# Optimization experiments

Hardware: AMD Instinct MI355X
Metric: run time of the kernel (lower is better)

The kernel has to match this reference:

```python
import jax, jax.numpy as jnp
import numpy as np
import math

T_SCALE = 99
FEAT_DIM = 400
BATCH = 2
C = 256
NH = 8
NS = 32
NSPB = 3
RATIO = 0.5
LOCAL_STEP = 33


def build_sample_mask(T=T_SCALE, ns=NS, nspb=NSPB, ratio=RATIO):
    # Vectorized port of _get_interp1d_mask. Flat layout: [time, (bin, start, end)].
    N = ns * nspb
    e_idx, s_idx = np.meshgrid(np.arange(T), np.arange(T), indexing='ij')
    valid = s_idx < e_idx
    starts_i = s_idx[valid].astype(np.int64)
    ends_i = e_idx[valid].astype(np.int64)
    starts = starts_i.astype(np.float64)
    ends = ends_i.astype(np.float64)
    center = ends - starts + 1.0
    xmin = starts - center * ratio
    plen = (ends + center * ratio) - xmin
    S = xmin[:, None] + (plen / (N - 1.0))[:, None] * np.arange(N)[None, :]  # [P, N]
    down = np.trunc(S).astype(np.int64)  # matches int(math.modf(s)[1]) (trunc toward 0)
    dec = S - down                       # can be negative when s < 0, as in the original
    up = np.ceil(S).astype(np.int64)
    bin_col = (np.arange(N) // nspb)[None, :] * (T * T) + (starts_i * T + ends_i)[:, None]
    M = np.zeros(T * ns * T * T, np.float64)
    vd = (down >= 0) & (down <= T - 1)
    np.add.at(M, (down * (ns * T * T) + bin_col)[vd], ((1.0 - dec) / nspb)[vd])
    vu = (up >= 0) & (up <= T - 1)
    np.add.at(M, (up * (ns * T * T) + bin_col)[vu], (dec / nspb)[vu])
    return M.reshape(T, ns * T * T).astype(np.float32)


def pos_ebb(scale, size):
    pos = jnp.arange(scale, dtype=jnp.float32)[:, None]
    div = jnp.exp(jnp.arange(0, size, 2, dtype=jnp.float32) * (-math.log(10000.0) / size))
    ang = pos * div
    # interleave sin (even) / cos (odd)
    return jnp.stack([jnp.sin(ang), jnp.cos(ang)], axis=-1).reshape(scale, size)


def layer_norm(x, g, b, eps=1e-5):
    mu = jnp.mean(x, -1, keepdims=True)
    var = jnp.mean((x - mu) ** 2, -1, keepdims=True)
    return (x - mu) * jax.lax.rsqrt(var + eps) * g + b


def mha(x, w_qkv, b_qkv, w_o, b_o, nh=NH):
    t, b, c = x.shape
    hd = c // nh
    q, k, v = jnp.split(x @ w_qkv.T + b_qkv, 3, axis=-1)
    q = q.reshape(t, b, nh, hd)
    k = k.reshape(t, b, nh, hd)
    v = v.reshape(t, b, nh, hd)
    att = jnp.einsum('qbhd,kbhd->bhqk', q, k) / math.sqrt(hd)
    att = jax.nn.softmax(att, axis=-1)
    o = jnp.einsum('bhqk,kbhd->qbhd', att, v).reshape(t, b, c)
    return o @ w_o.T + b_o


def encoder(x, p):
    # PyTorch post-norm TransformerEncoder (eval mode, dropout off) + final LayerNorm
    (qkv_w, qkv_b, o_w, o_b, l1_w, l1_b, l2_w, l2_b, n1_g, n1_b, n2_g, n2_b, nf_g, nf_b) = p
    for i in range(qkv_w.shape[0]):
        a = mha(x, qkv_w[i], qkv_b[i], o_w[i], o_b[i])
        x = layer_norm(x + a, n1_g[i], n1_b[i])
        f = jax.nn.relu(x @ l1_w[i].T + l1_b[i]) @ l2_w[i].T + l2_b[i]
        x = layer_norm(x + f, n2_g[i], n2_b[i])
    return layer_norm(x, nf_g, nf_b)


def conv1d(x, w, b, pad, groups=1):
    y = jax.lax.conv_general_dilated(x, w, (1,), [(pad, pad)],
                                     dimension_numbers=('NCH', 'OIH', 'NCH'),
                                     feature_group_count=groups)
    return y + b[None, :, None]


def conv2d(x, w, b, pad):
    y = jax.lax.conv_general_dilated(x, w, (1, 1), [(pad, pad), (pad, pad)],
                                     dimension_numbers=('NCHW', 'OIHW', 'NCHW'))
    return y + b[None, :, None, None]


def conv3d(x, w, b, stride):
    y = jax.lax.conv_general_dilated(x, w, stride, [(0, 0)] * 3,
                                     dimension_numbers=('NCDHW', 'OIDHW', 'NCDHW'))
    return y + b[None, :, None, None, None]


def _forward(x, cb_w, cb_b, tg_qkv_w, tg_qkv_b, tg_o_w, tg_o_b, tg_l1_w, tg_l1_b, tg_l2_w, tg_l2_b, tg_n1_g, tg_n1_b, tg_n2_g, tg_n2_b, tg_nf_g, tg_nf_b, tl_qkv_w, tl_qkv_b, tl_o_w, tl_o_b, tl_l1_w, tl_l1_b, tl_l2_w, tl_l2_b, tl_n1_g, tl_n1_b, tl_n2_g, tl_n2_b, tl_nf_g, tl_nf_b, s1_w, s1_b, s2_w, s2_b, c3_w, c3_b, p1_w, p1_b, p2_w, p2_b, p3_w, p3_b, sample_mask):
    B, _, T = x.shape
    base = jax.nn.relu(conv1d(x, cb_w, cb_b, pad=1, groups=4))  # [B,C,T]
    # local transformer on LOCAL_STEP-strided windows
    group = T // LOCAL_STEP
    tl_p = (tl_qkv_w, tl_qkv_b, tl_o_w, tl_o_b, tl_l1_w, tl_l1_b, tl_l2_w, tl_l2_b, tl_n1_g, tl_n1_b, tl_n2_g, tl_n2_b, tl_nf_g, tl_nf_b)
    feat = base.reshape(B, C, LOCAL_STEP, group).transpose(2, 3, 0, 1).reshape(LOCAL_STEP, B * group, C)
    feat = encoder(feat + pos_ebb(LOCAL_STEP, C)[:, None, :], tl_p)
    local = feat.reshape(LOCAL_STEP * group, B, C).transpose(1, 2, 0)  # [B,C,T]
    # global bidirectional transformer (shared weights, flipped second pass)
    tg_p = (tg_qkv_w, tg_qkv_b, tg_o_w, tg_o_b, tg_l1_w, tg_l1_b, tg_l2_w, tg_l2_b, tg_n1_g, tg_n1_b, tg_n2_g, tg_n2_b, tg_nf_g, tg_nf_b)
    g = base.transpose(2, 0, 1)  # [T,B,C]
    pe = pos_ebb(T, C)[:, None, :]
    f1 = encoder(g + pe, tg_p)
    f2 = encoder(g[::-1] + pe, tg_p)
    base2 = local + (f1 + f2[::-1]).transpose(1, 2, 0)  # [B,C,T]
    s = jax.nn.relu(conv1d(base2, s1_w, s1_b, pad=1, groups=4))
    start1 = jax.nn.sigmoid(conv1d(s, s2_w, s2_b, pad=0))[:, 0, :]  # [B,T]
    # boundary-matching layer: dense matmul against precomputed interp mask
    bm = jnp.matmul(base2, sample_mask).reshape(B, C, NS, T, T)
    p = jax.nn.relu(conv3d(bm, c3_w, c3_b, (NS, 1, 1)))[:, :, 0]  # [B,C,T,T]
    p = jax.nn.relu(conv2d(p, p1_w, p1_b, pad=1))
    p = jax.nn.relu(conv2d(p, p2_w, p2_b, pad=1))
    cm = jax.nn.sigmoid(conv2d(p, p3_w, p3_b, pad=0))  # [B,2,T,T]
    return cm, start1


def setup_inputs() -> dict:
    key = jax.random.key(0)
    ks = iter(jax.random.split(key, 80))
    def rnd(shape):
        return 0.02 * jax.random.normal(next(ks), shape, dtype=jnp.float32)
    inp = {'x': jax.random.normal(next(ks), (BATCH, FEAT_DIM, T_SCALE), dtype=jnp.float32)}
    inp['cb_w'] = rnd((C, FEAT_DIM // 4, 3)); inp['cb_b'] = jnp.zeros((C,), jnp.float32)
    for pre, n in (('tg', 6), ('tl', 3)):
        inp[pre + '_qkv_w'] = rnd((n, 3 * C, C)); inp[pre + '_qkv_b'] = jnp.zeros((n, 3 * C), jnp.float32)
        inp[pre + '_o_w'] = rnd((n, C, C)); inp[pre + '_o_b'] = jnp.zeros((n, C), jnp.float32)
        inp[pre + '_l1_w'] = rnd((n, 1024, C)); inp[pre + '_l1_b'] = jnp.zeros((n, 1024), jnp.float32)
        inp[pre + '_l2_w'] = rnd((n, C, 1024)); inp[pre + '_l2_b'] = jnp.zeros((n, C), jnp.float32)
        inp[pre + '_n1_g'] = jnp.ones((n, C), jnp.float32); inp[pre + '_n1_b'] = jnp.zeros((n, C), jnp.float32)
        inp[pre + '_n2_g'] = jnp.ones((n, C), jnp.float32); inp[pre + '_n2_b'] = jnp.zeros((n, C), jnp.float32)
        inp[pre + '_nf_g'] = jnp.ones((C,), jnp.float32); inp[pre + '_nf_b'] = jnp.zeros((C,), jnp.float32)
    inp['s1_w'] = rnd((C, C // 4, 3)); inp['s1_b'] = jnp.zeros((C,), jnp.float32)
    inp['s2_w'] = rnd((1, C, 1)); inp['s2_b'] = jnp.zeros((1,), jnp.float32)
    inp['c3_w'] = rnd((C, C, NS, 1, 1)); inp['c3_b'] = jnp.zeros((C,), jnp.float32)
    inp['p1_w'] = rnd((C, C, 3, 3)); inp['p1_b'] = jnp.zeros((C,), jnp.float32)
    inp['p2_w'] = rnd((C, C, 3, 3)); inp['p2_b'] = jnp.zeros((C,), jnp.float32)
    inp['p3_w'] = rnd((2, C, 1, 1)); inp['p3_b'] = jnp.zeros((2,), jnp.float32)
    inp['sample_mask'] = jnp.asarray(build_sample_mask())  # [T, NS*T*T], exact BMN interp mask
    return inp


def reference(x, cb_w, cb_b, tg_qkv_w, tg_qkv_b, tg_o_w, tg_o_b, tg_l1_w, tg_l1_b, tg_l2_w, tg_l2_b, tg_n1_g, tg_n1_b, tg_n2_g, tg_n2_b, tg_nf_g, tg_nf_b, tl_qkv_w, tl_qkv_b, tl_o_w, tl_o_b, tl_l1_w, tl_l1_b, tl_l2_w, tl_l2_b, tl_n1_g, tl_n1_b, tl_n2_g, tl_n2_b, tl_nf_g, tl_nf_b, s1_w, s1_b, s2_w, s2_b, c3_w, c3_b, p1_w, p1_b, p2_w, p2_b, p3_w, p3_b, sample_mask):
    return _forward(x, cb_w, cb_b, tg_qkv_w, tg_qkv_b, tg_o_w, tg_o_b, tg_l1_w, tg_l1_b, tg_l2_w, tg_l2_b, tg_n1_g, tg_n1_b, tg_n2_g, tg_n2_b, tg_nf_g, tg_nf_b, tl_qkv_w, tl_qkv_b, tl_o_w, tl_o_b, tl_l1_w, tl_l1_b, tl_l2_w, tl_l2_b, tl_n1_g, tl_n1_b, tl_n2_g, tl_n2_b, tl_nf_g, tl_nf_b, s1_w, s1_b, s2_w, s2_b, c3_w, c3_b, p1_w, p1_b, p2_w, p2_b, p3_w, p3_b, sample_mask)
```

## Files before the change

kernel.cpp:

```cpp
#include <hip/hip_runtime.h>
#include <math.h>

#define T99   99
#define CC    256
#define NHH   8
#define FEAT  400
#define NS_   32
#define LSTEP 33

typedef __attribute__((ext_vector_type(8))) short s8v;
typedef __attribute__((ext_vector_type(4))) float f4v;

__device__ __forceinline__ void mfma_bf16(f4v& d, s8v a, s8v b) {
  asm("v_mfma_f32_16x16x32_bf16 %0, %1, %2, %0" : "+v"(d) : "v"(a), "v"(b));
}

__device__ __forceinline__ unsigned short f2bf(float f) {
  union { float f; unsigned u; } x; x.f = f;
  unsigned r = x.u + 0x7FFFu + ((x.u >> 16) & 1u);
  return (unsigned short)(r >> 16);
}
__device__ __forceinline__ float bf2f(unsigned short h) {
  union { unsigned u; float f; } x; x.u = ((unsigned)h) << 16;
  return x.f;
}
__device__ __forceinline__ float blo(unsigned u) { union { unsigned x; float f; } c; c.x = u << 16; return c.f; }
__device__ __forceinline__ float bhi(unsigned u) { union { unsigned x; float f; } c; c.x = u & 0xffff0000u; return c.f; }

__device__ __forceinline__ float pe_val(int pos, int c) {
  int i = c >> 1;
  float freq = expf((float)(2 * i) * (-0.03597789207803197f));
  float ang = (float)pos * freq;
  return (c & 1) ? cosf(ang) : sinf(ang);
}

__global__ __launch_bounds__(128) void k_convbase(const float* __restrict__ x,
                                                  const float* __restrict__ w,
                                                  const float* __restrict__ bias,
                                                  float* __restrict__ base) {
  int b = blockIdx.x >> 8, co = blockIdx.x & 255, t = threadIdx.x;
  if (t >= T99) return;
  int g = co >> 6;
  float acc = bias[co];
  const float* xp = x + (size_t)(b * FEAT + g * 100) * T99;
  const float* wp = w + (size_t)co * 300;
  for (int ic = 0; ic < 100; ++ic) {
    float x0 = (t > 0)  ? xp[ic * T99 + t - 1] : 0.f;
    float x1 = xp[ic * T99 + t];
    float x2 = (t < 98) ? xp[ic * T99 + t + 1] : 0.f;
    acc += wp[ic * 3] * x0 + wp[ic * 3 + 1] * x1 + wp[ic * 3 + 2] * x2;
  }
  base[(size_t)(b * CC + co) * T99 + t] = fmaxf(acc, 0.f);
}

struct PackP {
  const float *gq, *go, *g1, *g2;
  const float *lq, *lo, *l1, *l2;
  const float *c3w, *p1w, *p2w;
  unsigned short *wtg, *wtl, *wog, *wol, *w3, *wba, *wbb;
};
#define S0 4718592
#define S1 2359296
#define S2 393216
#define S3 196608
#define S4 2097152
#define S5 589824
#define S6 589824
#define STOT (S0+S1+S2+S3+S4+S5+S6)

__device__ __forceinline__ float convW_val(const float* qkv, const float* o, const float* l1,
                                           const float* l2, int idx) {
  int l = idx / 786432, r = idx % 786432;
  if (r < 196608)      return qkv[(size_t)l * 196608 + r];
  else if (r < 262144) return o[(size_t)l * 65536 + (r - 196608)];
  else if (r < 524288) return l1[(size_t)l * 262144 + (r - 262144)];
  else                 return l2[(size_t)l * 262144 + (r - 524288)];
}
__device__ __forceinline__ float wb2_val(const float* pw, int idx) {
  int v8 = idx >> 3, j = idx & 7;
  int lane = v8 & 63, cog = (v8 >> 6) & 15, kst = (v8 >> 10) & 7, tap = v8 >> 13;
  int co = cog * 16 + (lane & 15);
  int k  = kst * 32 + (lane >> 4) * 8;
  return pw[((size_t)co * 256 + k + j) * 9 + tap];
}

__global__ __launch_bounds__(256) void k_pack(PackP P) {
  for (int idx = blockIdx.x * 256 + threadIdx.x; idx < STOT; idx += gridDim.x * 256) {
    int r = idx;
    if (r < S0) { P.wtg[r] = f2bf(convW_val(P.gq, P.go, P.g1, P.g2, r)); continue; }
    r -= S0;
    if (r < S1) { P.wtl[r] = f2bf(convW_val(P.lq, P.lo, P.l1, P.l2, r)); continue; }
    r -= S1;
    if (r < S2) { int l = r >> 16, q = r & 65535; int ci = q >> 8, co = q & 255;
                  P.wog[r] = f2bf(P.go[(size_t)l * 65536 + co * 256 + ci]); continue; }
    r -= S2;
    if (r < S3) { int l = r >> 16, q = r & 65535; int ci = q >> 8, co = q & 255;
                  P.wol[r] = f2bf(P.lo[(size_t)l * 65536 + co * 256 + ci]); continue; }
    r -= S3;
    if (r < S4) { int ci = r & 255, co = (r >> 8) & 255, n = r >> 16;
                  P.w3[r] = f2bf(P.c3w[((size_t)(co << 8) + ci) * 32 + n]); continue; }
    r -= S4;
    if (r < S5) { P.wba[r] = f2bf(wb2_val(P.p1w, r)); continue; }
    r -= S5;
    P.wbb[r] = f2bf(wb2_val(P.p2w, r));
  }
}

__global__ __launch_bounds__(256) void k_build2(const float* __restrict__ base,
                                                float* __restrict__ xl, unsigned short* __restrict__ xlb,
                                                float* __restrict__ xg, unsigned short* __restrict__ xgb) {
  int tid = threadIdx.x;
  if (blockIdx.z == 0) {
    if (blockIdx.x >= 198) return;
    int idx = blockIdx.x * 256 + tid;
    int ls = idx / 1536, r = idx % 1536, j = r >> 8, c = r & 255;
    int g = j >> 1, b = j & 1, t = ls * 3 + g;
    float v = base[(size_t)(b * CC + c) * T99 + t] + pe_val(ls, c);
    xl[idx] = v; xlb[idx] = f2bf(v);
  } else {
    int idx = blockIdx.x * 256 + tid;
    int t = idx >> 10, r = idx & 1023, b4 = r >> 8, c = r & 255;
    float v = (b4 < 2) ? base[(size_t)(b4 * CC + c) * T99 + t]
                       : base[(size_t)((b4 - 2) * CC + c) * T99 + (98 - t)];
    v += pe_val(t, c);
    xg[idx] = v; xgb[idx] = f2bf(v);
  }
}

struct GJ {
  const unsigned short* Ab;
  const unsigned short* W;
  const float* bias;
  const float* R;
  float* Yf;
  unsigned short* Yb;
  int M, N, K, flags;
};

__device__ void g_body(const GJ& j, int m0, int n0) {
  __shared__ __align__(16) unsigned short Al[64][40];
  __shared__ __align__(16) unsigned short Bl[64][40];
  int tid = threadIdx.x;
  int lane = tid & 63, w = tid >> 6, wm = w >> 1, wn = w & 1;
  int sp = tid >> 2, kc = (tid & 3) << 3;
  f4v acc[2][2];
#pragma unroll
  for (int mt = 0; mt < 2; ++mt)
#pragma unroll
    for (int nt = 0; nt < 2; ++nt) acc[mt][nt] = (f4v){0.f, 0.f, 0.f, 0.f};

  for (int k0 = 0; k0 < j.K; k0 += 32) {
    s8v av = {0, 0, 0, 0, 0, 0, 0, 0};
    int row = m0 + sp;
    if (row < j.M) av = *(const s8v*)&j.Ab[(size_t)row * j.K + k0 + kc];
    *(s8v*)&Al[sp][kc] = av;
    *(s8v*)&Bl[sp][kc] = *(const s8v*)&j.W[(size_t)(n0 + sp) * j.K + k0 + kc];
    __syncthreads();
    s8v af[2], bf[2];
#pragma unroll
    for (int mt = 0; mt < 2; ++mt)
      af[mt] = *(const s8v*)&Al[wm * 32 + mt * 16 + (lane & 15)][(lane >> 4) * 8];
#pragma unroll
    for (int nt = 0; nt < 2; ++nt)
      bf[nt] = *(const s8v*)&Bl[wn * 32 + nt * 16 + (lane & 15)][(lane >> 4) * 8];
#pragma unroll
    for (int mt = 0; mt < 2; ++mt)
#pragma unroll
      for (int nt = 0; nt < 2; ++nt) mfma_bf16(acc[mt][nt], af[mt], bf[nt]);
    __syncthreads();
  }
  asm volatile("s_nop 7\n\ts_nop 7\n\ts_nop 4");
#pragma unroll
  for (int mt = 0; mt < 2; ++mt) {
#pragma unroll
    for (int nt = 0; nt < 2; ++nt) {
      int col = n0 + wn * 32 + nt * 16 + (lane & 15);
      float bv = j.bias[col];
#pragma unroll
      for (int r = 0; r < 4; ++r) {
        int row = m0 + wm * 32 + mt * 16 + (lane >> 4) * 4 + r;
        if (row < j.M) {
          float v = acc[mt][nt][r] + bv;
          if (j.flags & 2) v += j.R[(size_t)row * j.N + col];
          if (j.flags & 1) v = fmaxf(v, 0.f);
          if (!(j.flags & 8)) j.Yf[(size_t)row * j.N + col] = v;
          if (j.flags & 4) j.Yb[(size_t)row * j.N + col] = f2bf(v);
        }
      }
    }
  }
}

__global__ __launch_bounds__(256) void k_g(GJ j) {
  if ((int)blockIdx.x * 64 >= j.M) return;
  g_body(j, blockIdx.x * 64, blockIdx.y * 64);
}

__global__ __launch_bounds__(256) void k_g2(GJ j0, GJ j1) {
  if (blockIdx.z == 0) {
    if ((int)blockIdx.x * 64 >= j0.M) return;
    g_body(j0, blockIdx.x * 64, blockIdx.y * 64);
  } else {
    if ((int)blockIdx.x * 64 >= j1.M) return;
    g_body(j1, blockIdx.x * 64, blockIdx.y * 64);
  }
}

__device__ void apl_body(const unsigned short* __restrict__ qkvb,
                         const unsigned short* __restrict__ Wt,
                         const float* __restrict__ ob,
                         const float* __restrict__ g, const float* __restrict__ beta,
                         float* __restrict__ X, unsigned short* __restrict__ Xb,
                         int T_, int B_, int tok) {
  __shared__ float qrow[256];
  __shared__ float sc[8][100];
  __shared__ float den[8];
  __shared__ float att[256];
  __shared__ float rs[256], rq[256];
  int tid = threadIdx.x;
  int b = tok % B_;
  qrow[tid] = bf2f(qkvb[(size_t)tok * 768 + tid]);
  __syncthreads();
  for (int e = tid; e < 8 * T_; e += 256) {
    int h = e / T_, k = e % T_;
    const unsigned short* kp = qkvb + (size_t)(k * B_ + b) * 768 + 256 + h * 32;
    float d = 0.f;
#pragma unroll
    for (int i = 0; i < 32; ++i) d += qrow[h * 32 + i] * bf2f(kp[i]);
    sc[h][k] = d * 0.176776695296636881f;
  }
  __syncthreads();
  int h = tid >> 5, lane = tid & 31;
  float m = -1e30f;
  for (int k = lane; k < T_; k += 32) m = fmaxf(m, sc[h][k]);
#pragma unroll
  for (int msk = 16; msk >= 1; msk >>= 1) m = fmaxf(m, __shfl_xor(m, msk, 32));
  float sum = 0.f;
  for (int k = lane; k < T_; k += 32) {
    float p = expf(sc[h][k] - m);
    sc[h][k] = p; sum += p;
  }
#pragma unroll
  for (int msk = 16; msk >= 1; msk >>= 1) sum += __shfl_xor(sum, msk, 32);
  if (lane == 0) den[h] = sum;
  float o = 0.f;
  for (int k = 0; k < T_; ++k)
    o += sc[h][k] * bf2f(qkvb[(size_t)(k * B_ + b) * 768 + 512 + tid]);
  o /= den[h];
  att[tid] = o;
  __syncthreads();
  float acc = ob[tid];
#pragma unroll 8
  for (int ci = 0; ci < 256; ++ci) acc += att[ci] * bf2f(Wt[(size_t)ci * 256 + tid]);
  float v = acc + X[(size_t)tok * 256 + tid];
  rs[tid] = v; rq[tid] = v * v; __syncthreads();
  for (int oo = 128; oo > 0; oo >>= 1) { if (tid < oo) { rs[tid] += rs[tid + oo]; rq[tid] += rq[tid + oo]; } __syncthreads(); }
  float mu = rs[0] * (1.f / 256.f);
  float var = rq[0] * (1.f / 256.f) - mu * mu;
  float r = (v - mu) * rsqrtf(var + 1e-5f) * g[tid] + beta[tid];
  X[(size_t)tok * 256 + tid] = r;
  Xb[(size_t)tok * 256 + tid] = f2bf(r);
}

__global__ __launch_bounds__(256) void k_apl(const unsigned short* qkvb, const unsigned short* Wt,
                                             const float* ob, const float* g, const float* beta,
                                             float* X, unsigned short* Xb, int T_, int B_, int M) {
  if ((int)blockIdx.x >= M) return;
  apl_body(qkvb, Wt, ob, g, beta, X, Xb, T_, B_, blockIdx.x);
}

__global__ __launch_bounds__(256) void k_apl2(const unsigned short* q0, const unsigned short* Wt0,
                                              const float* ob0, const float* g0, const float* be0,
                                              float* X0, unsigned short* Xb0, int T0, int B0, int M0,
                                              const unsigned short* q1, const unsigned short* Wt1,
                                              const float* ob1, const float* g1, const float* be1,
                                              float* X1, unsigned short* Xb1, int T1, int B1, int M1) {
  int tok = blockIdx.x;
  if (blockIdx.z == 0) {
    if (tok >= M0) return;
    apl_body(q0, Wt0, ob0, g0, be0, X0, Xb0, T0, B0, tok);
  } else {
    if (tok >= M1) return;
    apl_body(q1, Wt1, ob1, g1, be1, X1, Xb1, T1, B1, tok);
  }
}

__device__ __forceinline__ void ln_body(const float* __restrict__ X, const float* __restrict__ g,
                                        const float* __restrict__ bb, float* __restrict__ Y,
                                        unsigned short* __restrict__ Yb, int tok) {
  __shared__ float rs[256], rq[256];
  int c = threadIdx.x;
  float v = X[(size_t)tok * 256 + c];
  rs[c] = v; rq[c] = v * v; __syncthreads();
  for (int o = 128; o > 0; o >>= 1) { if (c < o) { rs[c] += rs[c + o]; rq[c] += rq[c + o]; } __syncthreads(); }
  float mu = rs[0] * (1.f / 256.f);
  float var = rq[0] * (1.f / 256.f) - mu * mu;
  float r = (v - mu) * rsqrtf(var + 1e-5f) * g[c] + bb[c];
  Y[(size_t)tok * 256 + c] = r;
  if (Yb) Yb[(size_t)tok * 256 + c] = f2bf(r);
}

__global__ __launch_bounds__(256) void k_ln(const float* __restrict__ X, const float* __restrict__ g,
                                            const float* __restrict__ bb, float* __restrict__ Y,
                                            unsigned short* __restrict__ Yb) {
  ln_body(X, g, bb, Y, Yb, blockIdx.x);
}

__global__ __launch_bounds__(256) void k_ln2(const float* __restrict__ X0, const float* __restrict__ g0,
                                             const float* __restrict__ bb0, float* __restrict__ Y0,
                                             unsigned short* __restrict__ Yb0, int n0,
                                             const float* __restrict__ X1, const float* __restrict__ g1,
                                             const float* __restrict__ bb1, float* __restrict__ Y1,
                                             unsigned short* __restrict__ Yb1, int n1) {
  int tok = blockIdx.x;
  if (blockIdx.z == 0) { if (tok < n0) ln_body(X0, g0, bb0, Y0, Yb0, tok); }
  else                 { if (tok < n1) ln_body(X1, g1, bb1, Y1, Yb1, tok); }
}

__device__ __forceinline__ float ln3(float v, float* rs, float* rq) {
  int c = threadIdx.x;
  rs[c] = v; rq[c] = v * v; __syncthreads();
  for (int o = 128; o > 0; o >>= 1) { if (c < o) { rs[c] += rs[c + o]; rq[c] += rq[c + o]; } __syncthreads(); }
  float mu = rs[0] * (1.f / 256.f);
  float var = rq[0] * (1.f / 256.f) - mu * mu;
  float r = (v - mu) * rsqrtf(var + 1e-5f);
  __syncthreads();
  return r;
}

__global__ __launch_bounds__(256) void k_combine2(const float* __restrict__ XL, const float* __restrict__ XG,
                                                  const float* __restrict__ nfgL, const float* __restrict__ nfbL,
                                                  const float* __restrict__ nfgG, const float* __restrict__ nfbG,
                                                  float* __restrict__ base2, unsigned short* __restrict__ b2t) {
  __shared__ float rs[256], rq[256];
  int t = blockIdx.x % T99, b = blockIdx.x / T99, c = threadIdx.x;
  int ls = t / 3, g = t % 3;
  int tokL = ls * 6 + g * 2 + b;
  int tok1 = t * 4 + b;
  int tok2 = (98 - t) * 4 + 2 + b;
  float vL = ln3(XL[(size_t)tokL * 256 + c], rs, rq) * nfgL[c] + nfbL[c];
  float v1 = ln3(XG[(size_t)tok1 * 256 + c], rs, rq) * nfgG[c] + nfbG[c];
  float v2 = ln3(XG[(size_t)tok2 * 256 + c], rs, rq) * nfgG[c] + nfbG[c];
  float v = vL + v1 + v2;
  base2[((size_t)(b * CC) + c) * T99 + t] = v;
  b2t[((size_t)(b * T99) + t) * 256 + c] = f2bf(v);
}

__device__ void gm_body(const unsigned short* __restrict__ b2t, const unsigned short* __restrict__ w3tb,
                        unsigned short* __restrict__ Gb, int mi, int ni, int nb, bool padzero) {
  __shared__ __align__(16) unsigned short Al[64][40];
  __shared__ __align__(16) unsigned short Bl[64][40];
  int n = nb >> 1, b = nb & 1;
  int m0 = mi * 64, n0 = ni * 64;
  int tid = threadIdx.x;
  if (padzero)
    ((unsigned int*)(Gb + (size_t)NS_ * T99 * 512))[tid] = 0u;
  const unsigned short* A = b2t + (size_t)b * T99 * 256;
  const unsigned short* W = w3tb + (size_t)n * 65536;
  int lane = tid & 63, w = tid >> 6, wm = w >> 1, wn = w & 1;
  int sp = tid >> 2, kc = (tid & 3) << 3;
  f4v acc[2][2];
#pragma unroll
  for (int mt = 0; mt < 2; ++mt)
#pragma unroll
    for (int nt = 0; nt < 2; ++nt) acc[mt][nt] = (f4v){0.f, 0.f, 0.f, 0.f};
#pragma unroll
  for (int k0 = 0; k0 < 256; k0 += 32) {
    s8v av = {0, 0, 0, 0, 0, 0, 0, 0};
    int row = m0 + sp;
    if (row < T99) av = *(const s8v*)&A[(size_t)row * 256 + k0 + kc];
    *(s8v*)&Al[sp][kc] = av;
    *(s8v*)&Bl[sp][kc] = *(const s8v*)&W[(size_t)(n0 + sp) * 256 + k0 + kc];
    __syncthreads();
    s8v af[2], bf[2];
#pragma unroll
    for (int mt = 0; mt < 2; ++mt)
      af[mt] = *(const s8v*)&Al[wm * 32 + mt * 16 + (lane & 15)][(lane >> 4) * 8];
#pragma unroll
    for (int nt = 0; nt < 2; ++nt)
      bf[nt] = *(const s8v*)&Bl[wn * 32 + nt * 16 + (lane & 15)][(lane >> 4) * 8];
#pragma unroll
    for (int mt = 0; mt < 2; ++mt)
#pragma unroll
      for (int nt = 0; nt < 2; ++nt) mfma_bf16(acc[mt][nt], af[mt], bf[nt]);
    __syncthreads();
  }
  asm volatile("s_nop 7\n\ts_nop 7\n\ts_nop 4");
#pragma unroll
  for (int mt = 0; mt < 2; ++mt) {
#pragma unroll
    for (int nt = 0; nt < 2; ++nt) {
      int co = n0 + wn * 32 + nt * 16 + (lane & 15);
#pragma unroll
      for (int r = 0; r < 4; ++r) {
        int t = m0 + wm * 32 + mt * 16 + (lane >> 4) * 4 + r;
        if (t < T99)
          Gb[((size_t)(n * T99 + t) * 256 + co) * 2 + b] = f2bf(acc[mt][nt][r]);
      }
    }
  }
}

__device__ void sfuse_body(const float* __restrict__ base2, const float* __restrict__ s1w,
                           const float* __restrict__ s1b, const float* __restrict__ s2w,
                           const float* __restrict__ s2b, float* __restrict__ out, int bid) {
  __shared__ float rs[256];
  int b = bid / T99, t = bid % T99, co = threadIdx.x;
  int g = co >> 6;
  float acc = s1b[co];
  const float* xp = base2 + (size_t)(b * CC + g * 64) * T99;
  const float* wp = s1w + (size_t)co * 192;
  for (int ic = 0; ic < 64; ++ic) {
    float x0 = (t > 0)  ? xp[ic * T99 + t - 1] : 0.f;
    float x1 = xp[ic * T99 + t];
    float x2 = (t < 98) ? xp[ic * T99 + t + 1] : 0.f;
    acc += wp[ic * 3] * x0 + wp[ic * 3 + 1] * x1 + wp[ic * 3 + 2] * x2;
  }
  rs[co] = fmaxf(acc, 0.f) * s2w[co];
  __syncthreads();
  for (int o = 128; o > 0; o >>= 1) { if (co < o) rs[co] += rs[co + o]; __syncthreads(); }
  if (co == 0) out[bid] = 1.f / (1.f + expf(-(rs[0] + s2b[0])));
}

__global__ __launch_bounds__(256) void k_gmsf(const unsigned short* b2t, const unsigned short* w3tb,
                                              unsigned short* Gb,
                                              const float* base2, const float* s1w, const float* s1b,
                                              const float* s2w, const float* s2b, float* sout) {
  int bid = blockIdx.x;
  if (bid < 512) {
    int mi = bid & 1, ni = (bid >> 1) & 3, nb = bid >> 3;
    gm_body(b2t, w3tb, Gb, mi, ni, nb, bid == 0);
  } else {
    sfuse_body(base2, s1w, s1b, s2w, s2b, sout, bid - 512);
  }
}

__global__ __launch_bounds__(256) void k_ppre(const unsigned short* __restrict__ Gb,
                                              const float* __restrict__ c3b,
                                              unsigned int* __restrict__ pinb32) {
  __shared__ float w0s[96], w1s[96];
  __shared__ int   ofs[96];
  __shared__ float part[128][4];
  int e = blockIdx.x % T99, s = blockIdx.x / T99;
  int tid = threadIdx.x;
  if (s >= e) {
    if (tid < 128) {
      float z0 = fmaxf(c3b[2 * tid], 0.f), z1 = fmaxf(c3b[2 * tid + 1], 0.f);
      unsigned int zz = ((unsigned)f2bf(z1) << 16) | (unsigned)f2bf(z0);
      pinb32[((size_t)s * T99 + e) * 128 + tid] = zz;
      pinb32[((size_t)(T99 + s) * T99 + e) * 128 + tid] = zz;
    }
    return;
  }
  if (tid < 96) {
    double center = (double)(e - s + 1);
    double S = ((double)s - 0.5 * center) + ((2.0 * center - 1.0) / 95.0) * (double)tid;
    double dn = trunc(S);
    double dec = S - dn;
    int di = (int)dn;
    double uc = ceil(S);
    int ui = (int)uc;
    int n = tid / 3;
    float w0 = 0.f, w1 = 0.f;
    int r0 = 0;
    if (dn >= 0.0 && dn <= 98.0) {
      r0 = di;
      w0 = (float)((1.0 - dec) / 3.0);
      if (uc >= 0.0 && uc <= 98.0) {
        if (ui == di) w0 += (float)(dec / 3.0);
        else          w1  = (float)(dec / 3.0);
      }
    }
    w0s[tid] = w0; w1s[tid] = w1;
    ofs[tid] = (n * T99 + r0) * 1024;
  }
  __syncthreads();
  int ch = tid & 127, half = tid >> 7;
  float a00 = 0.f, a01 = 0.f, a10 = 0.f, a11 = 0.f;
  const char* basep = (const char*)Gb + ch * 8;
  int k0 = half * 48;
#pragma unroll 8
  for (int k = k0; k < k0 + 48; ++k) {
    float w0 = w0s[k], w1 = w1s[k];
    const uint2* p = (const uint2*)(basep + ofs[k]);
    uint2 u0 = p[0];
    uint2 u1 = p[128];
    a00 += w0 * blo(u0.x) + w1 * blo(u1.x);
    a01 += w0 * bhi(u0.x) + w1 * bhi(u1.x);
    a10 += w0 * blo(u0.y) + w1 * blo(u1.y);
    a11 += w0 * bhi(u0.y) + w1 * bhi(u1.y);
  }
  if (half) { part[ch][0] = a00; part[ch][1] = a01; part[ch][2] = a10; part[ch][3] = a11; }
  __syncthreads();
  if (tid < 128) {
    a00 += part[ch][0]; a01 += part[ch][1]; a10 += part[ch][2]; a11 += part[ch][3];
    float b0 = c3b[2 * tid], b1 = c3b[2 * tid + 1];
    unsigned int zb0 = ((unsigned)f2bf(fmaxf(a10 + b1, 0.f)) << 16) | (unsigned)f2bf(fmaxf(a00 + b0, 0.f));
    unsigned int zb1 = ((unsigned)f2bf(fmaxf(a11 + b1, 0.f)) << 16) | (unsigned)f2bf(fmaxf(a01 + b0, 0.f));
    pinb32[((size_t)s * T99 + e) * 128 + tid] = zb0;
    pinb32[((size_t)(T99 + s) * T99 + e) * 128 + tid] = zb1;
  }
}

__global__ __launch_bounds__(256) void k_cvec(const float* __restrict__ pw, const float* __restrict__ cin,
                                              const float* __restrict__ bias, int reluCin,
                                              float* __restrict__ coutF, unsigned short* __restrict__ coutB) {
  __shared__ float rs[256];
  int co = blockIdx.x, ci = threadIdx.x;
  float c = cin[ci];
  if (reluCin) c = fmaxf(c, 0.f);
  const float* wp = pw + ((size_t)co * 256 + ci) * 9;
  float wsum = 0.f;
#pragma unroll
  for (int t = 0; t < 9; ++t) wsum += wp[t];
  rs[ci] = wsum * c;
  __syncthreads();
  for (int o = 128; o > 0; o >>= 1) { if (ci < o) rs[ci] += rs[ci + o]; __syncthreads(); }
  if (ci == 0) {
    float r = fmaxf(bias[co] + rs[0], 0.f);
    coutF[co] = r;
    coutB[co] = f2bf(r);
  }
}

__device__ __forceinline__ int aoff(int s) {
  int tap = s >> 3, kst = s & 7;
  return ((tap / 3) * 10 + (tap % 3)) * 264 + kst * 32;
}
__device__ __forceinline__ void ldb4(const unsigned short* __restrict__ B0, int s, s8v* dst) {
#pragma unroll
  for (int nt = 0; nt < 4; ++nt) dst[nt] = *(const s8v*)(B0 + (size_t)s * 8192 + nt * 512);
}

__global__ __launch_bounds__(256) void k_conv3x3(const unsigned short* __restrict__ in,
                                                 const unsigned short* __restrict__ wbf,
                                                 const float* __restrict__ bias,
                                                 const unsigned short* __restrict__ cvecB,
                                                 int D, int lo, int hi,
                                                 unsigned short* __restrict__ out) {
  __shared__ __align__(16) unsigned short Ah[100 * 264];
  int b = blockIdx.z;
  int co0 = blockIdx.y * 128;
  int ti = blockIdx.x / 13, tj = blockIdx.x % 13;
  int i0 = ti * 8, j0 = tj * 8;
  int tid = threadIdx.x;

  if (i0 - 1 >= lo && i0 + 8 <= hi && j0 - 1 >= lo && j0 + 8 <= hi && i0 - 1 >= j0 + 8 + D) {
    const unsigned int* cv = (const unsigned int*)(cvecB + co0);
    unsigned int* ob = (unsigned int*)out;
#pragma unroll
    for (int r = 0; r < 16; ++r) {
      int idx = r * 256 + tid;
      int sp = idx >> 6, cp = idx & 63;
      int gi = i0 + (sp >> 3), gj = j0 + (sp & 7);
      ob[((size_t)(b * T99 + gi) * T99 + gj) * 128 + (co0 >> 1) + cp] = cv[cp];
    }
    return;
  }

#pragma unroll
  for (int it = 0; it < 13; ++it) {
    int chunk = it * 256 + tid;
    if (chunk < 3200) {
      int row = chunk >> 5;
      int cc = (chunk & 31) * 8;
      int gi = i0 + row / 10 - 1, gj = j0 + row % 10 - 1;
      s8v val = {0, 0, 0, 0, 0, 0, 0, 0};
      if (gi >= 0 && gi < T99 && gj >= 0 && gj < T99)
        val = *(const s8v*)&in[((size_t)(b * T99 + gi) * T99 + gj) * 256 + cc];
      *(s8v*)&Ah[row * 264 + cc] = val;
    }
  }
  __syncthreads();

  int lane = tid & 63, w = tid >> 6, wm = w >> 1, wn = w & 1;
  int l15 = lane & 15, lk = lane >> 4;
  int spL0 = wm * 32 + l15, spL1 = spL0 + 16;
  int hr0 = (spL0 >> 3) * 10 + (spL0 & 7);
  int hr1 = (spL1 >> 3) * 10 + (spL1 & 7);
  const unsigned short* A0 = &Ah[hr0 * 264 + lk * 8];
  const unsigned short* A1 = &Ah[hr1 * 264 + lk * 8];
  int cogbase = blockIdx.y * 8 + wn * 4;
  const unsigned short* B0 = wbf + (size_t)cogbase * 512 + (size_t)lane * 8;

  f4v acc[2][4];
#pragma unroll
  for (int mt = 0; mt < 2; ++mt)
#pragma unroll
    for (int nt = 0; nt < 4; ++nt) acc[mt][nt] = (f4v){0.f, 0.f, 0.f, 0.f};

  s8v a0c, a1c, a0n, a1n;
  s8v bq[3][4];
  a0c = *(const s8v*)(A0 + aoff(0));
  a1c = *(const s8v*)(A1 + aoff(0));
  a0n = a0c; a1n = a1c;
  ldb4(B0, 0, bq[0]);
  ldb4(B0, 1, bq[1]);
#pragma unroll
  for (int s = 0; s < 72; ++s) {
    if (s + 2 < 72) ldb4(B0, s + 2, bq[(s + 2) % 3]);
    if (s + 1 < 72) {
      a0n = *(const s8v*)(A0 + aoff(s + 1));
      a1n = *(const s8v*)(A1 + aoff(s + 1));
    }
#pragma unroll
    for (int nt = 0; nt < 4; ++nt) {
      mfma_bf16(acc[0][nt], a0c, bq[s % 3][nt]);
      mfma_bf16(acc[1][nt], a1c, bq[s % 3][nt]);
    }
    a0c = a0n; a1c = a1n;
  }

  asm volatile("s_nop 7\n\ts_nop 7\n\ts_nop 4");
#pragma unroll
  for (int mt = 0; mt < 2; ++mt) {
#pragma unroll
    for (int nt = 0; nt < 4; ++nt) {
      int co = co0 + wn * 64 + nt * 16 + l15;
      float bv = bias[co];
#pragma unroll
      for (int r = 0; r < 4; ++r) {
        int sp = wm * 32 + mt * 16 + lk * 4 + r;
        int gi = i0 + (sp >> 3), gj = j0 + (sp & 7);
        if (gi < T99 && gj < T99) {
          float v = fmaxf(acc[mt][nt][r] + bv, 0.f);
          out[((size_t)(b * T99 + gi) * T99 + gj) * 256 + co] = f2bf(v);
        }
      }
    }
  }
}

__global__ __launch_bounds__(256) void k_p3(const unsigned short* __restrict__ p2o,
                                            const float* __restrict__ w, const float* __restrict__ bias,
                                            float* __restrict__ cm) {
  int idx = blockIdx.x * 256 + threadIdx.x;
  if (idx >= 2 * T99 * T99) return;
  int j = idx % T99, i = (idx / T99) % T99, b = idx / (T99 * T99);
  float a0 = bias[0], a1 = bias[1];
  const unsigned short* row = p2o + ((size_t)(b * T99 + i) * T99 + j) * 256;
  for (int c8 = 0; c8 < 256; c8 += 8) {
    s8v v = *(const s8v*)&row[c8];
#pragma unroll
    for (int q = 0; q < 8; ++q) {
      float x = bf2f((unsigned short)v[q]);
      a0 += w[c8 + q] * x;
      a1 += w[256 + c8 + q] * x;
    }
  }
  size_t base = (size_t)b * 2 * T99 * T99 + (size_t)i * T99 + j;
  cm[base] = 1.f / (1.f + expf(-a0));
  cm[base + T99 * T99] = 1.f / (1.f + expf(-a1));
}

struct EncW {
  const float *qkvw, *qkvb, *ow, *ob, *l1w, *l1b, *l2w, *l2b, *n1g, *n1b, *n2g, *n2b, *nfg, *nfb;
};
struct EncBufs {
  float* x; unsigned short* xb;
  float* yb;
  unsigned short *qkvb, *hb;
  int M;
};

static GJ jqkv(const EncW& W, const unsigned short* Wb, int l, const EncBufs& B) {
  GJ j = {}; j.Ab = B.xb; j.W = Wb + (size_t)l * 786432;
  j.bias = W.qkvb + (size_t)l * 768; j.Yb = B.qkvb; j.flags = 4 | 8;
  j.M = B.M; j.N = 768; j.K = 256; return j;
}
static GJ jffn1(const EncW& W, const unsigned short* Wb, int l, const EncBufs& B) {
  GJ j = {}; j.Ab = B.xb; j.W = Wb + (size_t)l * 786432 + 262144;
  j.bias = W.l1b + (size_t)l * 1024; j.Yb = B.hb; j.flags = 1 | 4 | 8;
  j.M = B.M; j.N = 1024; j.K = 256; return j;
}
static GJ jffn2(const EncW& W, const unsigned short* Wb, int l, const EncBufs& B) {
  GJ j = {}; j.Ab = B.hb; j.W = Wb + (size_t)l * 786432 + 524288;
  j.bias = W.l2b + (size_t)l * 256; j.R = B.x; j.Yf = B.yb; j.flags = 2;
  j.M = B.M; j.N = 256; j.K = 1024; return j;
}

extern "C" void kernel_launch(void* const* d_in, const int* in_sizes, int n_in,
                              void* d_out, int out_size, void* d_ws, size_t ws_size,
                              hipStream_t stream) {
  (void)in_sizes; (void)n_in; (void)out_size; (void)ws_size;
  const float* x    = (const float*)d_in[0];
  const float* cbw  = (const float*)d_in[1];
  const float* cbb  = (const float*)d_in[2];
  EncW tg = {(const float*)d_in[3],  (const float*)d_in[4],  (const float*)d_in[5],  (const float*)d_in[6],
             (const float*)d_in[7],  (const float*)d_in[8],  (const float*)d_in[9],  (const float*)d_in[10],
             (const float*)d_in[11], (const float*)d_in[12], (const float*)d_in[13], (const float*)d_in[14],
             (const float*)d_in[15], (const float*)d_in[16]};
  EncW tl = {(const float*)d_in[17], (const float*)d_in[18], (const float*)d_in[19], (const float*)d_in[20],
             (const float*)d_in[21], (const float*)d_in[22], (const float*)d_in[23], (const float*)d_in[24],
             (const float*)d_in[25], (const float*)d_in[26], (const float*)d_in[27], (const float*)d_in[28],
             (const float*)d_in[29], (const float*)d_in[30]};
  const float* s1w = (const float*)d_in[31];
  const float* s1b = (const float*)d_in[32];
  const float* s2w = (const float*)d_in[33];
  const float* s2b = (const float*)d_in[34];
  const float* c3w = (const float*)d_in[35];
  const float* c3b = (const float*)d_in[36];
  const float* p1w = (const float*)d_in[37];
  const float* p1b = (const float*)d_in[38];
  const float* p2w = (const float*)d_in[39];
  const float* p2b = (const float*)d_in[40];
  const float* p3w = (const float*)d_in[41];
  const float* p3b = (const float*)d_in[42];

  float* outp = (float*)d_out;

  char* wp = (char*)d_ws;
  auto alloc = [&](size_t bytes) -> void* {
    void* p = (void*)wp;
    wp += (bytes + 255) & ~(size_t)255;
    return p;
  };
  float* base  = (float*)alloc(sizeof(float) * 2 * CC * T99);
  const int ML = 198, MG = 396;
  EncBufs BG, BL;
  BG.M = MG; BL.M = ML;
  BG.x  = (float*)alloc(sizeof(float) * MG * 256);
  BL.x  = (float*)alloc(sizeof(float) * ML * 256);
  BG.xb = (unsigned short*)alloc(sizeof(short) * MG * 256);
  BL.xb = (unsigned short*)alloc(sizeof(short) * ML * 256);
  BG.yb = (float*)alloc(sizeof(float) * MG * 256);
  BL.yb = (float*)alloc(sizeof(float) * ML * 256);
  BG.qkvb = (unsigned short*)alloc(sizeof(short) * MG * 768);
  BL.qkvb = (unsigned short*)alloc(sizeof(short) * ML * 768);
  BG.hb = (unsigned short*)alloc(sizeof(short) * MG * 1024);
  BL.hb = (unsigned short*)alloc(sizeof(short) * ML * 1024);
  float* base2 = (float*)alloc(sizeof(float) * 2 * CC * T99);
  unsigned short* b2t = (unsigned short*)alloc(sizeof(short) * 2 * T99 * 256);
  unsigned short* w3tb = (unsigned short*)alloc(sizeof(short) * 32 * 256 * 256);
  unsigned short* Gb = (unsigned short*)alloc(sizeof(short) * (2 * NS_ * T99 * 256 + 512));
  unsigned short* pinb = (unsigned short*)alloc(sizeof(short) * 2 * T99 * T99 * 256);
  unsigned short* p1o  = (unsigned short*)alloc(sizeof(short) * 2 * T99 * T99 * 256);
  unsigned short* p2o  = (unsigned short*)alloc(sizeof(short) * 2 * T99 * T99 * 256);
  unsigned short* wb2a = (unsigned short*)alloc(sizeof(short) * 9 * 256 * 256);
  unsigned short* wb2b = (unsigned short*)alloc(sizeof(short) * 9 * 256 * 256);
  unsigned short* wtgb = (unsigned short*)alloc(sizeof(short) * 6 * 786432);
  unsigned short* wtlb = (unsigned short*)alloc(sizeof(short) * 3 * 786432);
  unsigned short* wotg = (unsigned short*)alloc(sizeof(short) * 6 * 65536);
  unsigned short* wotl = (unsigned short*)alloc(sizeof(short) * 3 * 65536);
  float* c1F = (float*)alloc(sizeof(float) * 256);
  unsigned short* c1B = (unsigned short*)alloc(sizeof(short) * 256);
  float* c2F = (float*)alloc(sizeof(float) * 256);
  unsigned short* c2B = (unsigned short*)alloc(sizeof(short) * 256);

  PackP PK = {tg.qkvw, tg.ow, tg.l1w, tg.l2w, tl.qkvw, tl.ow, tl.l1w, tl.l2w,
              c3w, p1w, p2w, wtgb, wtlb, wotg, wotl, w3tb, wb2a, wb2b};
  k_pack<<<dim3(8192), dim3(256), 0, stream>>>(PK);
  k_cvec<<<dim3(256), dim3(256), 0, stream>>>(p1w, c3b, p1b, 1, c1F, c1B);
  k_cvec<<<dim3(256), dim3(256), 0, stream>>>(p2w, c1F, p2b, 0, c2F, c2B);
  k_convbase<<<dim3(512), dim3(128), 0, stream>>>(x, cbw, cbb, base);
  k_build2<<<dim3(396, 1, 2), dim3(256), 0, stream>>>(base, BL.x, BL.xb, BG.x, BG.xb);

  const int mgG = 7;
  for (int l = 0; l < 3; ++l) {
    k_g2<<<dim3(mgG, 12, 2), dim3(256), 0, stream>>>(jqkv(tl, wtlb, l, BL), jqkv(tg, wtgb, l, BG));
    k_apl2<<<dim3(MG, 1, 2), dim3(256), 0, stream>>>(
        BL.qkvb, wotl + (size_t)l * 65536, tl.ob + l * 256, tl.n1g + l * 256, tl.n1b + l * 256,
        BL.x, BL.xb, LSTEP, 6, ML,
        BG.qkvb, wotg + (size_t)l * 65536, tg.ob + l * 256, tg.n1g + l * 256, tg.n1b + l * 256,
        BG.x, BG.xb, T99, 4, MG);
    k_g2<<<dim3(mgG, 16, 2), dim3(256), 0, stream>>>(jffn1(tl, wtlb, l, BL), jffn1(tg, wtgb, l, BG));
    k_g2<<<dim3(mgG, 4, 2), dim3(256), 0, stream>>>(jffn2(tl, wtlb, l, BL), jffn2(tg, wtgb, l, BG));
    k_ln2<<<dim3(MG, 1, 2), dim3(256), 0, stream>>>(BL.yb, tl.n2g + l * 256, tl.n2b + l * 256, BL.x, BL.xb, ML,
                                                    BG.yb, tg.n2g + l * 256, tg.n2b + l * 256, BG.x, BG.xb, MG);
  }
  for (int l = 3; l < 6; ++l) {
    k_g<<<dim3(mgG, 12), dim3(256), 0, stream>>>(jqkv(tg, wtgb, l, BG));
    k_apl<<<dim3(MG), dim3(256), 0, stream>>>(BG.qkvb, wotg + (size_t)l * 65536, tg.ob + l * 256,
                                              tg.n1g + l * 256, tg.n1b + l * 256, BG.x, BG.xb, T99, 4, MG);
    k_g<<<dim3(mgG, 16), dim3(256), 0, stream>>>(jffn1(tg, wtgb, l, BG));
    k_g<<<dim3(mgG, 4), dim3(256), 0, stream>>>(jffn2(tg, wtgb, l, BG));
    k_ln<<<dim3(MG), dim3(256), 0, stream>>>(BG.yb, tg.n2g + l * 256, tg.n2b + l * 256, BG.x, BG.xb);
  }
  k_combine2<<<dim3(198), dim3(256), 0, stream>>>(BL.x, BG.x, tl.nfg, tl.nfb, tg.nfg, tg.nfb, base2, b2t);
  k_gmsf<<<dim3(710), dim3(256), 0, stream>>>(b2t, w3tb, Gb, base2, s1w, s1b, s2w, s2b,
                                              outp + 2 * 2 * T99 * T99);
  k_ppre<<<dim3(T99 * T99), dim3(256), 0, stream>>>(Gb, c3b, (unsigned int*)pinb);
  k_conv3x3<<<dim3(169, 2, 2), dim3(256), 0, stream>>>(pinb, wb2a, p1b, c1B, 0, 0, 98, p1o);
  k_conv3x3<<<dim3(169, 2, 2), dim3(256), 0, stream>>>(p1o, wb2b, p2b, c2B, 2, 1, 97, p2o);
  k_p3<<<dim3(77), dim3(256), 0, stream>>>(p2o, p3w, p3b, outp);
}
```

Baseline: 608.3 us.

## Fuse FFN second linear with residual add and LayerNorm per token

Replaces the MFMA GEMM for the FFN down-projection plus the separate LayerNorm kernel with one per-token kernel. Each block loads a hidden row into shared memory, does a scalar dot product against a transposed bf16 W2 (packed in k_pack), adds bias and residual, then applies LayerNorm. This removes one launch per layer and the fp32 intermediate buffer. In exchange it gives up tensor-core math and re-reads the full 512KB weight matrix once per token, which may be memory-bound.

```diff
diff --git a/kernel.cpp b/kernel.cpp
--- a/kernel.cpp
+++ b/kernel.cpp
@@ -57,7 +57,7 @@
   const float *gq, *go, *g1, *g2;
   const float *lq, *lo, *l1, *l2;
   const float *c3w, *p1w, *p2w;
-  unsigned short *wtg, *wtl, *wog, *wol, *w3, *wba, *wbb;
+  unsigned short *wtg, *wtl, *wog, *wol, *w3, *wba, *wbb, *w2g, *w2l;
 };
 #define S0 4718592
 #define S1 2359296
@@ -66,7 +66,9 @@
 #define S4 2097152
 #define S5 589824
 #define S6 589824
-#define STOT (S0+S1+S2+S3+S4+S5+S6)
+#define S7 1572864
+#define S8 786432
+#define STOT (S0+S1+S2+S3+S4+S5+S6+S7+S8)
 
 __device__ __forceinline__ float convW_val(const float* qkv, const float* o, const float* l1,
                                            const float* l2, int idx) {
@@ -82,6 +84,10 @@
   int co = cog * 16 + (lane & 15);
   int k  = kst * 32 + (lane >> 4) * 8;
   return pw[((size_t)co * 256 + k + j) * 9 + tap];
+}
+__device__ __forceinline__ float w2t_val(const float* l2, int idx) {
+  int n = idx & 255, k = (idx >> 8) & 1023, l = idx >> 18;
+  return l2[(size_t)l * 262144 + n * 1024 + k];
 }
 
 __global__ __launch_bounds__(256) void k_pack(PackP P) {
@@ -102,7 +108,11 @@
     r -= S4;
     if (r < S5) { P.wba[r] = f2bf(wb2_val(P.p1w, r)); continue; }
     r -= S5;
-    P.wbb[r] = f2bf(wb2_val(P.p2w, r));
+    if (r < S6) { P.wbb[r] = f2bf(wb2_val(P.p2w, r)); continue; }
+    r -= S6;
+    if (r < S7) { P.w2g[r] = f2bf(w2t_val(P.g2, r)); continue; }
+    r -= S7;
+    P.w2l[r] = f2bf(w2t_val(P.l2, r));
   }
 }
 
@@ -285,36 +295,50 @@
   }
 }
 
-__device__ __forceinline__ void ln_body(const float* __restrict__ X, const float* __restrict__ g,
-                                        const float* __restrict__ bb, float* __restrict__ Y,
-                                        unsigned short* __restrict__ Yb, int tok) {
+__device__ void fl_body(const unsigned short* __restrict__ hb, const unsigned short* __restrict__ W2t,
+                        const float* __restrict__ b2, const float* __restrict__ g,
+                        const float* __restrict__ beta,
+                        float* __restrict__ X, unsigned short* __restrict__ Xb, int tok) {
+  __shared__ float hrow[1024];
   __shared__ float rs[256], rq[256];
-  int c = threadIdx.x;
-  float v = X[(size_t)tok * 256 + c];
-  rs[c] = v; rq[c] = v * v; __syncthreads();
-  for (int o = 128; o > 0; o >>= 1) { if (c < o) { rs[c] += rs[c + o]; rq[c] += rq[c + o]; } __syncthreads(); }
+  int tid = threadIdx.x;
+  for (int k = tid; k < 1024; k += 256) hrow[k] = bf2f(hb[(size_t)tok * 1024 + k]);
+  __syncthreads();
+  float acc = b2[tid];
+  const unsigned short* w = W2t + tid;
+#pragma unroll 8
+  for (int k = 0; k < 1024; ++k) acc += hrow[k] * bf2f(w[(size_t)k * 256]);
+  float v = acc + X[(size_t)tok * 256 + tid];
+  rs[tid] = v; rq[tid] = v * v; __syncthreads();
+  for (int o = 128; o > 0; o >>= 1) { if (tid < o) { rs[tid] += rs[tid + o]; rq[tid] += rq[tid + o]; } __syncthreads(); }
   float mu = rs[0] * (1.f / 256.f);
   float var = rq[0] * (1.f / 256.f) - mu * mu;
-  float r = (v - mu) * rsqrtf(var + 1e-5f) * g[c] + bb[c];
-  Y[(size_t)tok * 256 + c] = r;
-  if (Yb) Yb[(size_t)tok * 256 + c] = f2bf(r);
-}
-
-__global__ __launch_bounds__(256) void k_ln(const float* __restrict__ X, const float* __restrict__ g,
-                                            const float* __restrict__ bb, float* __restrict__ Y,
-                                            unsigned short* __restrict__ Yb) {
-  ln_body(X, g, bb, Y, Yb, blockIdx.x);
-}
-
-__global__ __launch_bounds__(256) void k_ln2(const float* __restrict__ X0, const float* __restrict__ g0,
-                                             const float* __restrict__ bb0, float* __restrict__ Y0,
-                                             unsigned short* __restrict__ Yb0, int n0,
-                                             const float* __restrict__ X1, const float* __restrict__ g1,
-                                             const float* __restrict__ bb1, float* __restrict__ Y1,
-                                             unsigned short* __restrict__ Yb1, int n1) {
+  float r = (v - mu) * rsqrtf(var + 1e-5f) * g[tid] + beta[tid];
+  X[(size_t)tok * 256 + tid] = r;
+  Xb[(size_t)tok * 256 + tid] = f2bf(r);
+}
+
+__global__ __launch_bounds__(256) void k_fl(const unsigned short* hb, const unsigned short* W2t,
+                                            const float* b2, const float* g, const float* beta,
+                                            float* X, unsigned short* Xb, int M) {
+  if ((int)blockIdx.x >= M) return;
+  fl_body(hb, W2t, b2, g, beta, X, Xb, blockIdx.x);
+}
+
+__global__ __launch_bounds__(256) void k_fl2(const unsigned short* h0, const unsigned short* W0,
+                                             const float* b0, const float* g0, const float* be0,
+                                             float* X0, unsigned short* Xb0, int M0,
+                                             const unsigned short* h1, const unsigned short* W1,
+                                             const float* b1, const float* g1, const float* be1,
+                                             float* X1, unsigned short* Xb1, int M1) {
   int tok = blockIdx.x;
-  if (blockIdx.z == 0) { if (tok < n0) ln_body(X0, g0, bb0, Y0, Yb0, tok); }
-  else                 { if (tok < n1) ln_body(X1, g1, bb1, Y1, Yb1, tok); }
+  if (blockIdx.z == 0) {
+    if (tok >= M0) return;
+    fl_body(h0, W0, b0, g0, be0, X0, Xb0, tok);
+  } else {
+    if (tok >= M1) return;
+    fl_body(h1, W1, b1, g1, be1, X1, Xb1, tok);
+  }
 }
 
 __device__ __forceinline__ float ln3(float v, float* rs, float* rq) {
@@ -658,7 +682,6 @@
 };
 struct EncBufs {
   float* x; unsigned short* xb;
-  float* yb;
   unsigned short *qkvb, *hb;
   int M;
 };
@@ -672,11 +695,6 @@
   GJ j = {}; j.Ab = B.xb; j.W = Wb + (size_t)l * 786432 + 262144;
   j.bias = W.l1b + (size_t)l * 1024; j.Yb = B.hb; j.flags = 1 | 4 | 8;
   j.M = B.M; j.N = 1024; j.K = 256; return j;
-}
-static GJ jffn2(const EncW& W, const unsigned short* Wb, int l, const EncBufs& B) {
-  GJ j = {}; j.Ab = B.hb; j.W = Wb + (size_t)l * 786432 + 524288;
-  j.bias = W.l2b + (size_t)l * 256; j.R = B.x; j.Yf = B.yb; j.flags = 2;
-  j.M = B.M; j.N = 256; j.K = 1024; return j;
 }
 
 extern "C" void kernel_launch(void* const* d_in, const int* in_sizes, int n_in,
@@ -723,8 +741,6 @@
   BL.x  = (float*)alloc(sizeof(float) * ML * 256);
   BG.xb = (unsigned short*)alloc(sizeof(short) * MG * 256);
   BL.xb = (unsigned short*)alloc(sizeof(short) * ML * 256);
-  BG.yb = (float*)alloc(sizeof(float) * MG * 256);
-  BL.yb = (float*)alloc(sizeof(float) * ML * 256);
   BG.qkvb = (unsigned short*)alloc(sizeof(short) * MG * 768);
   BL.qkvb = (unsigned short*)alloc(sizeof(short) * ML * 768);
   BG.hb = (unsigned short*)alloc(sizeof(short) * MG * 1024);
@@ -742,13 +758,15 @@
   unsigned short* wtlb = (unsigned short*)alloc(sizeof(short) * 3 * 786432);
   unsigned short* wotg = (unsigned short*)alloc(sizeof(short) * 6 * 65536);
   unsigned short* wotl = (unsigned short*)alloc(sizeof(short) * 3 * 65536);
+  unsigned short* w2tg = (unsigned short*)alloc(sizeof(short) * 6 * 262144);
+  unsigned short* w2tl = (unsigned short*)alloc(sizeof(short) * 3 * 262144);
   float* c1F = (float*)alloc(sizeof(float) * 256);
   unsigned short* c1B = (unsigned short*)alloc(sizeof(short) * 256);
   float* c2F = (float*)alloc(sizeof(float) * 256);
   unsigned short* c2B = (unsigned short*)alloc(sizeof(short) * 256);
 
   PackP PK = {tg.qkvw, tg.ow, tg.l1w, tg.l2w, tl.qkvw, tl.ow, tl.l1w, tl.l2w,
-              c3w, p1w, p2w, wtgb, wtlb, wotg, wotl, w3tb, wb2a, wb2b};
+              c3w, p1w, p2w, wtgb, wtlb, wotg, wotl, w3tb, wb2a, wb2b, w2tg, w2tl};
   k_pack<<<dim3(8192), dim3(256), 0, stream>>>(PK);
   k_cvec<<<dim3(256), dim3(256), 0, stream>>>(p1w, c3b, p1b, 1, c1F, c1B);
   k_cvec<<<dim3(256), dim3(256), 0, stream>>>(p2w, c1F, p2b, 0, c2F, c2B);
@@ -764,17 +782,19 @@
         BG.qkvb, wotg + (size_t)l * 65536, tg.ob + l * 256, tg.n1g + l * 256, tg.n1b + l * 256,
         BG.x, BG.xb, T99, 4, MG);
     k_g2<<<dim3(mgG, 16, 2), dim3(256), 0, stream>>>(jffn1(tl, wtlb, l, BL), jffn1(tg, wtgb, l, BG));
-    k_g2<<<dim3(mgG, 4, 2), dim3(256), 0, stream>>>(jffn2(tl, wtlb, l, BL), jffn2(tg, wtgb, l, BG));
-    k_ln2<<<dim3(MG, 1, 2), dim3(256), 0, stream>>>(BL.yb, tl.n2g + l * 256, tl.n2b + l * 256, BL.x, BL.xb, ML,
-                                                    BG.yb, tg.n2g + l * 256, tg.n2b + l * 256, BG.x, BG.xb, MG);
+    k_fl2<<<dim3(MG, 1, 2), dim3(256), 0, stream>>>(
+        BL.hb, w2tl + (size_t)l * 262144, tl.l2b + l * 256, tl.n2g + l * 256, tl.n2b + l * 256,
+        BL.x, BL.xb, ML,
+        BG.hb, w2tg + (size_t)l * 262144, tg.l2b + l * 256, tg.n2g + l * 256, tg.n2b + l * 256,
+        BG.x, BG.xb, MG);
   }
   for (int l = 3; l < 6; ++l) {
     k_g<<<dim3(mgG, 12), dim3(256), 0, stream>>>(jqkv(tg, wtgb, l, BG));
     k_apl<<<dim3(MG), dim3(256), 0, stream>>>(BG.qkvb, wotg + (size_t)l * 65536, tg.ob + l * 256,
                                               tg.n1g + l * 256, tg.n1b + l * 256, BG.x, BG.xb, T99, 4, MG);
     k_g<<<dim3(mgG, 16), dim3(256), 0, stream>>>(jffn1(tg, wtgb, l, BG));
-    k_g<<<dim3(mgG, 4), dim3(256), 0, stream>>>(jffn2(tg, wtgb, l, BG));
-    k_ln<<<dim3(MG), dim3(256), 0, stream>>>(BG.yb, tg.n2g + l * 256, tg.n2b + l * 256, BG.x, BG.xb);
+    k_fl<<<dim3(MG), dim3(256), 0, stream>>>(BG.hb, w2tg + (size_t)l * 262144, tg.l2b + l * 256,
+                                             tg.n2g + l * 256, tg.n2b + l * 256, BG.x, BG.xb, MG);
   }
   k_combine2<<<dim3(198), dim3(256), 0, stream>>>(BL.x, BG.x, tl.nfg, tl.nfb, tg.nfg, tg.nfb, base2, b2t);
   k_gmsf<<<dim3(710), dim3(256), 0, stream>>>(b2t, w3tb, Gb, base2, s1w, s1b, s2w, s2b,
```

After: 734.7 us. 20.8% more time.
